# Kernel optimization log

Measured on AMD Instinct MI355X. Metric: run time of the kernel, lower is better.

The kernel has to match this reference:

```python
import jax, jax.numpy as jnp
import numpy as np

BS, QLEN, DIM, H = 2, 2048, 2048, 16
DH = DIM // H


def setup_inputs() -> dict:
    key = jax.random.key(0)
    ks = jax.random.split(key, 10)
    s = 0.02
    return {
        "input": jax.random.normal(ks[0], (BS, QLEN, DIM), jnp.float32),
        "mask": jnp.ones((BS, QLEN), jnp.int32),
        "wq": jax.random.normal(ks[1], (DIM, DIM), jnp.float32) * s,
        "bq": jax.random.normal(ks[2], (DIM,), jnp.float32) * s,
        "wk": jax.random.normal(ks[3], (DIM, DIM), jnp.float32) * s,
        "bk": jax.random.normal(ks[4], (DIM,), jnp.float32) * s,
        "wv": jax.random.normal(ks[5], (DIM, DIM), jnp.float32) * s,
        "bv": jax.random.normal(ks[6], (DIM,), jnp.float32) * s,
        "wo": jax.random.normal(ks[7], (DIM, DIM), jnp.float32) * s,
        "bo": jax.random.normal(ks[8], (DIM,), jnp.float32) * s,
    }


def _shape(x, bs):
    # (bs, len, dim) -> (bs, H, len, DH)
    return x.reshape(bs, -1, H, DH).transpose(0, 2, 1, 3)


def reference(input, mask, wq, bq, wk, bk, wv, bv, wo, bo):
    bs, qlen, dim = input.shape
    # torch Linear: y = x @ W.T + b
    q = _shape(input @ wq.T + bq, bs)  # (bs,H,q,dh)
    k = _shape(input @ wk.T + bk, bs)  # (bs,H,k,dh)
    v = _shape(input @ wv.T + bv, bs)  # (bs,H,k,dh)
    q = q / jnp.sqrt(jnp.asarray(DH, q.dtype))
    scores = jnp.einsum("bhqd,bhkd->bhqk", q, k)
    # mask (bs, klen): positions where mask==0 are masked with -inf
    neg = (mask == 0)[:, None, None, :]  # (bs,1,1,klen)
    scores = jnp.where(neg, -jnp.inf, scores)
    weights = jax.nn.softmax(scores.astype(jnp.float32), axis=-1).astype(scores.dtype)
    # dropout p=0 (eval): identity
    context = jnp.einsum("bhqk,bhkd->bhqd", weights, v)
    context = context.transpose(0, 2, 1, 3).reshape(bs, qlen, dim)
    return context @ wo.T + bo
```

## Files before the change

### kernel.cpp

```cpp
#include <hip/hip_runtime.h>
#include <hip/hip_bf16.h>

#define BS 2
#define QLEN 2048
#define DIM 2048
#define H 16
#define DH 128
#define MTOT (BS*QLEN)

#define BM 256
#define BN 128
#define BK 64
#define NT (DIM/BK)

typedef __hip_bfloat16 bf16;
using f32x4 = __attribute__((ext_vector_type(4))) float;
using s16x8 = __attribute__((ext_vector_type(8))) short;

__device__ inline void gload_lds16(const bf16* g, bf16* l) {
    __builtin_amdgcn_global_load_lds(
        (const __attribute__((address_space(1))) void*)g,
        (__attribute__((address_space(3))) void*)l,
        16, 0, 0);
}

__global__ __launch_bounds__(256) void cast6(
    const float* __restrict__ x,
    const float* __restrict__ w0, const float* __restrict__ w1,
    const float* __restrict__ w2, const float* __restrict__ w3,
    bf16* xo, bf16* o0, bf16* o1, bf16* o2, bf16* o3, int n4)
{
    const float* in; bf16* out;
    switch (blockIdx.y) {
        case 0:  in = w0; out = o0; break;
        case 1:  in = w1; out = o1; break;
        case 2:  in = w2; out = o2; break;
        case 3:  in = w3; out = o3; break;
        case 4:  in = x;        out = xo;        break;
        default: in = x + 4*(size_t)n4; out = xo + 4*(size_t)n4; break;
    }
    int i = blockIdx.x * 256 + threadIdx.x;
    if (i < n4) {
        float4 v = ((const float4*)in)[i];
        __hip_bfloat162 p0 = __float22bfloat162_rn(make_float2(v.x, v.y));
        __hip_bfloat162 p1 = __float22bfloat162_rn(make_float2(v.z, v.w));
        ((__hip_bfloat162*)out)[2*i]   = p0;
        ((__hip_bfloat162*)out)[2*i+1] = p1;
    }
}

__global__ __launch_bounds__(512, 2) void gemm_qk(
    const bf16* __restrict__ A,
    const bf16* __restrict__ Wq, const bf16* __restrict__ Wk,
    const float* __restrict__ bq, const float* __restrict__ bk,
    bf16* __restrict__ Qo, bf16* __restrict__ Ko,
    float qscale)
{
    __shared__ __align__(16) bf16 smem[2*256*64*2];
    bf16* const SA = smem;
    bf16* const SB = smem + 2*256*64;

    const int t = threadIdx.x;
    const int lane = t & 63, w = t >> 6;
    const int row16 = lane & 15, quad = lane >> 4;

    const int sid = (blockIdx.z * 16 + blockIdx.y) * 8 + blockIdx.x;
    const int swz = (sid & 7) * 32 + (sid >> 3);
    const int zz = swz >> 7;
    const int m0 = ((swz >> 3) & 15) * 256;
    const int n0 = (swz & 7) * 256;
    const int mo = (w >> 2) * 128, no = (w & 3) * 64;

    const bf16*  Bw   = (zz == 0) ? Wq : Wk;
    const float* bias = (zz == 0) ? bq : bk;
    const float  scale = (zz == 0) ? qscale : 1.0f;

    auto stageA_part = [&](int kt, int bufi, int h) {
        bf16* dst = SA + bufi * (256*64);
        #pragma unroll
        for (int i = 0; i < 2; i++) {
            int c = i*512 + t;
            int rp = c >> 3, g = c & 7;
            int row = (rp & 63) + ((rp & 64) << 1) + h*64;
            int src = g ^ (row & 7);
            gload_lds16(A + (size_t)(m0 + row) * DIM + kt + src*8, dst + (row*8 + g)*8);
        }
    };
    auto stageB_half = [&](int kt, int bufi, int h) {
        bf16* dst = SB + bufi * (256*64);
        #pragma unroll
        for (int i = 0; i < 2; i++) {
            int c = i*512 + t;
            int rp = c >> 3, g = c & 7;
            int row = rp + h*128;
            int src = g ^ (row & 7);
            gload_lds16(Bw + (size_t)(n0 + row) * DIM + kt + src*8, dst + (row*8 + g)*8);
        }
    };

    f32x4 acc[8][4];
    #pragma unroll
    for (int i = 0; i < 8; i++)
        #pragma unroll
        for (int j = 0; j < 4; j++)
            acc[i][j] = (f32x4){0.f, 0.f, 0.f, 0.f};

    stageB_half(0, 0, 0); stageB_half(0, 0, 1);
    stageA_part(0, 0, 0); stageA_part(0, 0, 1);
    asm volatile("s_waitcnt vmcnt(0)" ::: "memory");
    __builtin_amdgcn_s_barrier();
    asm volatile("" ::: "memory");

    for (int J = 0; J < NT; ++J) {
        const bf16* Asb = SA + (J & 1) * (256*64);
        const bf16* Bsb = SB + (J & 1) * (256*64);
        const int stbuf = (J + 1) & 1;
        const bool st = (J + 1 < NT);
        s16x8 bfr[4][2];

        #pragma unroll
        for (int p = 0; p < 4; ++p) {
            s16x8 af[2][2];
            #pragma unroll
            for (int i = 0; i < 2; i++)
                #pragma unroll
                for (int kk = 0; kk < 2; kk++)
                    af[i][kk] = *(const s16x8*)&Asb[(mo + (2*p+i)*16 + row16)*64 +
                                                    (((kk*4+quad) ^ (row16&7)))*8];
            if (p == 0) {
                #pragma unroll
                for (int nj = 0; nj < 4; nj++)
                    #pragma unroll
                    for (int kk = 0; kk < 2; kk++)
                        bfr[nj][kk] = *(const s16x8*)&Bsb[(no + nj*16 + row16)*64 +
                                                          (((kk*4+quad) ^ (row16&7)))*8];
            }
            if (st) {
                if      (p == 0) stageB_half((J+1)*BK, stbuf, 0);
                else if (p == 1) stageB_half((J+1)*BK, stbuf, 1);
                else if (p == 2) stageA_part((J+1)*BK, stbuf, 0);
                else             stageA_part((J+1)*BK, stbuf, 1);
            }
            if (p == 1) {
                if (J < NT-1) asm volatile("s_waitcnt vmcnt(4)" ::: "memory");
                else          asm volatile("s_waitcnt vmcnt(0)" ::: "memory");
            }
            if (p == 3 && J < NT-1)
                asm volatile("s_waitcnt vmcnt(2)" ::: "memory");

            asm volatile("" ::: "memory");
            __builtin_amdgcn_s_barrier();
            asm volatile("s_waitcnt lgkmcnt(0)" ::: "memory");
            __builtin_amdgcn_sched_barrier(0);
            __builtin_amdgcn_s_setprio(1);
            #pragma unroll
            for (int kk = 0; kk < 2; kk++)
                #pragma unroll
                for (int i = 0; i < 2; i++)
                    #pragma unroll
                    for (int nj = 0; nj < 4; nj++)
                        acc[2*p+i][nj] = __builtin_amdgcn_mfma_f32_16x16x32_bf16(
                            af[i][kk], bfr[nj][kk], acc[2*p+i][nj], 0, 0, 0);
            __builtin_amdgcn_s_setprio(0);
            if (!(p == 3 && J == NT-1)) {
                asm volatile("" ::: "memory");
                __builtin_amdgcn_s_barrier();
                asm volatile("" ::: "memory");
            }
        }
    }

    bf16* out = (zz == 0) ? Qo : Ko;
    #pragma unroll
    for (int mi = 0; mi < 8; mi++)
        #pragma unroll
        for (int nj = 0; nj < 4; nj++) {
            int n = n0 + no + nj*16 + row16;
            float bv_ = bias[n];
            #pragma unroll
            for (int r = 0; r < 4; r++) {
                int m = m0 + mo + mi*16 + quad*4 + r;
                out[(size_t)m * DIM + n] = __float2bfloat16((acc[mi][nj][r] + bv_) * scale);
            }
        }
}

__global__ __launch_bounds__(512, 2) void gemm_v(
    const bf16* __restrict__ A, const bf16* __restrict__ B,
    const float* __restrict__ bias, bf16* __restrict__ Vo)
{
    __shared__ __align__(16) bf16 smem[3*BM*BK + 3*BN*BK];
    bf16* const SA = smem;
    bf16* const SB = smem + 3*BM*BK;

    const int t = threadIdx.x;
    const int lane = t & 63, w = t >> 6;
    const int row16 = lane & 15, quad = lane >> 4;
    const int sid = blockIdx.y * gridDim.x + blockIdx.x;
    const int swz = (sid & 7) * 32 + (sid >> 3);
    const int m0 = (swz >> 4) * BM, n0 = (swz & 15) * BN;
    const int mo = (w >> 1) * 64, no = (w & 1) * 64;

    auto stageA = [&](int kt, int bufi) {
        bf16* dst = SA + bufi * (BM*BK);
        #pragma unroll
        for (int i = 0; i < 4; i++) {
            int idx = i*512 + t;
            int row = idx >> 3, g = idx & 7;
            int src = g ^ (row & 7);
            gload_lds16(A + (size_t)(m0 + row) * DIM + kt + src*8, dst + idx*8);
        }
    };
    auto stageB = [&](int kt, int bufi) {
        bf16* dst = SB + bufi * (BN*BK);
        #pragma unroll
        for (int i = 0; i < 2; i++) {
            int idx = i*512 + t;
            int row = idx >> 3, g = idx & 7;
            int src = g ^ (row & 7);
            gload_lds16(B + (size_t)(n0 + row) * DIM + kt + src*8, dst + idx*8);
        }
    };

    f32x4 acc[4][4];
    for (int i = 0; i < 4; i++)
        for (int j = 0; j < 4; j++)
            acc[i][j] = (f32x4){0.f, 0.f, 0.f, 0.f};

    stageA(0,    0); stageB(0,    0);
    stageA(BK,   1); stageB(BK,   1);
    stageA(2*BK, 2); stageB(2*BK, 2);
    asm volatile("s_waitcnt vmcnt(12)" ::: "memory");
    __builtin_amdgcn_s_barrier();
    asm volatile("" ::: "memory");

    int buf = 0;
    for (int J = 0; J < NT; ++J) {
        const bf16* Asb = SA + buf * (BM*BK);
        const bf16* Bsb = SB + buf * (BN*BK);

        s16x8 af0[4], bf0[4];
        #pragma unroll
        for (int mt = 0; mt < 4; mt++)
            af0[mt] = *(const s16x8*)&Asb[(mo + mt*16 + row16)*BK + ((quad ^ (row16&7)))*8];
        #pragma unroll
        for (int nt = 0; nt < 4; nt++)
            bf0[nt] = *(const s16x8*)&Bsb[(no + nt*16 + row16)*BK + ((quad ^ (row16&7)))*8];
        if (J >= 1 && J + 2 < NT) {
            int sl = (buf == 0) ? 2 : buf - 1;
            stageA((J+2)*BK, sl); stageB((J+2)*BK, sl);
        }
        asm volatile("" ::: "memory");
        __builtin_amdgcn_s_barrier();
        asm volatile("s_waitcnt lgkmcnt(0)" ::: "memory");
        __builtin_amdgcn_sched_barrier(0);
        __builtin_amdgcn_s_setprio(1);
        #pragma unroll
        for (int mt = 0; mt < 4; mt++)
            #pragma unroll
            for (int nt = 0; nt < 4; nt++)
                acc[mt][nt] = __builtin_amdgcn_mfma_f32_16x16x32_bf16(
                    af0[mt], bf0[nt], acc[mt][nt], 0, 0, 0);
        __builtin_amdgcn_s_setprio(0);
        asm volatile("" ::: "memory");
        __builtin_amdgcn_s_barrier();
        asm volatile("" ::: "memory");

        s16x8 af1[4], bf1[4];
        #pragma unroll
        for (int mt = 0; mt < 4; mt++)
            af1[mt] = *(const s16x8*)&Asb[(mo + mt*16 + row16)*BK + (((4+quad) ^ (row16&7)))*8];
        #pragma unroll
        for (int nt = 0; nt < 4; nt++)
            bf1[nt] = *(const s16x8*)&Bsb[(no + nt*16 + row16)*BK + (((4+quad) ^ (row16&7)))*8];
        asm volatile("" ::: "memory");
        __builtin_amdgcn_s_barrier();
        asm volatile("s_waitcnt lgkmcnt(0)" ::: "memory");
        __builtin_amdgcn_sched_barrier(0);
        __builtin_amdgcn_s_setprio(1);
        #pragma unroll
        for (int mt = 0; mt < 4; mt++)
            #pragma unroll
            for (int nt = 0; nt < 4; nt++)
                acc[mt][nt] = __builtin_amdgcn_mfma_f32_16x16x32_bf16(
                    af1[mt], bf1[nt], acc[mt][nt], 0, 0, 0);
        __builtin_amdgcn_s_setprio(0);
        if (J < NT-2)
            asm volatile("s_waitcnt vmcnt(6)" ::: "memory");
        else if (J == NT-2)
            asm volatile("s_waitcnt vmcnt(0)" ::: "memory");
        if (J < NT-1) {
            asm volatile("" ::: "memory");
            __builtin_amdgcn_s_barrier();
            asm volatile("" ::: "memory");
        }
        buf = (buf == 2) ? 0 : buf + 1;
    }

    __syncthreads();
    bf16* Ts = smem;
    for (int mt = 0; mt < 4; mt++)
        for (int nt = 0; nt < 4; nt++) {
            int nn = no + nt*16 + row16;
            float bv_ = bias[n0 + nn];
            for (int r = 0; r < 4; r++) {
                int mm = mo + mt*16 + quad*4 + r;
                Ts[nn*264 + mm] = __float2bfloat16(acc[mt][nt][r] + bv_);
            }
        }
    __syncthreads();
    const int b = m0 >> 11, q0b = m0 & 2047;
    #pragma unroll
    for (int i = 0; i < 8; i++) {
        int chunk = i*512 + t;
        int row = chunk >> 5;
        int c = chunk & 31;
        s16x8 val = *(const s16x8*)&Ts[row*264 + c*8];
        *(s16x8*)(Vo + ((size_t)(b*DIM + n0 + row))*QLEN + q0b + c*8) = val;
    }
}

__global__ __launch_bounds__(512, 2) void gemm_out(
    const bf16* __restrict__ A, const bf16* __restrict__ B,
    const float* __restrict__ bias, float* __restrict__ out)
{
    __shared__ __align__(16) bf16 smem[3*BM*BK + 3*BN*BK];
    bf16* const SA = smem;
    bf16* const SB = smem + 3*BM*BK;

    const int t = threadIdx.x;
    const int lane = t & 63, w = t >> 6;
    const int row16 = lane & 15, quad = lane >> 4;
    const int sid = blockIdx.y * gridDim.x + blockIdx.x;
    const int swz = (sid & 7) * 32 + (sid >> 3);
    const int m0 = (swz >> 4) * BM, n0 = (swz & 15) * BN;
    const int mo = (w >> 1) * 64, no = (w & 1) * 64;

    auto stageA = [&](int kt, int bufi) {
        bf16* dst = SA + bufi * (BM*BK);
        #pragma unroll
        for (int i = 0; i < 4; i++) {
            int idx = i*512 + t;
            int row = idx >> 3, g = idx & 7;
            int src = g ^ (row & 7);
            gload_lds16(A + (size_t)(m0 + row) * DIM + kt + src*8, dst + idx*8);
        }
    };
    auto stageB = [&](int kt, int bufi) {
        bf16* dst = SB + bufi * (BN*BK);
        #pragma unroll
        for (int i = 0; i < 2; i++) {
            int idx = i*512 + t;
            int row = idx >> 3, g = idx & 7;
            int src = g ^ (row & 7);
            gload_lds16(B + (size_t)(n0 + row) * DIM + kt + src*8, dst + idx*8);
        }
    };

    f32x4 acc[4][4];
    for (int i = 0; i < 4; i++)
        for (int j = 0; j < 4; j++)
            acc[i][j] = (f32x4){0.f, 0.f, 0.f, 0.f};

    stageA(0,    0); stageB(0,    0);
    stageA(BK,   1); stageB(BK,   1);
    stageA(2*BK, 2); stageB(2*BK, 2);
    asm volatile("s_waitcnt vmcnt(12)" ::: "memory");
    __builtin_amdgcn_s_barrier();
    asm volatile("" ::: "memory");

    int buf = 0;
    for (int J = 0; J < NT; ++J) {
        const bf16* Asb = SA + buf * (BM*BK);
        const bf16* Bsb = SB + buf * (BN*BK);

        s16x8 af0[4], bf0[4];
        #pragma unroll
        for (int mt = 0; mt < 4; mt++)
            af0[mt] = *(const s16x8*)&Asb[(mo + mt*16 + row16)*BK + ((quad ^ (row16&7)))*8];
        #pragma unroll
        for (int nt = 0; nt < 4; nt++)
            bf0[nt] = *(const s16x8*)&Bsb[(no + nt*16 + row16)*BK + ((quad ^ (row16&7)))*8];
        if (J >= 1 && J + 2 < NT) {
            int sl = (buf == 0) ? 2 : buf - 1;
            stageA((J+2)*BK, sl); stageB((J+2)*BK, sl);
        }
        asm volatile("" ::: "memory");
        __builtin_amdgcn_s_barrier();
        asm volatile("s_waitcnt lgkmcnt(0)" ::: "memory");
        __builtin_amdgcn_sched_barrier(0);
        __builtin_amdgcn_s_setprio(1);
        #pragma unroll
        for (int mt = 0; mt < 4; mt++)
            #pragma unroll
            for (int nt = 0; nt < 4; nt++)
                acc[mt][nt] = __builtin_amdgcn_mfma_f32_16x16x32_bf16(
                    af0[mt], bf0[nt], acc[mt][nt], 0, 0, 0);
        __builtin_amdgcn_s_setprio(0);
        asm volatile("" ::: "memory");
        __builtin_amdgcn_s_barrier();
        asm volatile("" ::: "memory");

        s16x8 af1[4], bf1[4];
        #pragma unroll
        for (int mt = 0; mt < 4; mt++)
            af1[mt] = *(const s16x8*)&Asb[(mo + mt*16 + row16)*BK + (((4+quad) ^ (row16&7)))*8];
        #pragma unroll
        for (int nt = 0; nt < 4; nt++)
            bf1[nt] = *(const s16x8*)&Bsb[(no + nt*16 + row16)*BK + (((4+quad) ^ (row16&7)))*8];
        asm volatile("" ::: "memory");
        __builtin_amdgcn_s_barrier();
        asm volatile("s_waitcnt lgkmcnt(0)" ::: "memory");
        __builtin_amdgcn_sched_barrier(0);
        __builtin_amdgcn_s_setprio(1);
        #pragma unroll
        for (int mt = 0; mt < 4; mt++)
            #pragma unroll
            for (int nt = 0; nt < 4; nt++)
                acc[mt][nt] = __builtin_amdgcn_mfma_f32_16x16x32_bf16(
                    af1[mt], bf1[nt], acc[mt][nt], 0, 0, 0);
        __builtin_amdgcn_s_setprio(0);
        if (J < NT-2)
            asm volatile("s_waitcnt vmcnt(6)" ::: "memory");
        else if (J == NT-2)
            asm volatile("s_waitcnt vmcnt(0)" ::: "memory");
        if (J < NT-1) {
            asm volatile("" ::: "memory");
            __builtin_amdgcn_s_barrier();
            asm volatile("" ::: "memory");
        }
        buf = (buf == 2) ? 0 : buf + 1;
    }

    for (int mt = 0; mt < 4; mt++)
        for (int nt = 0; nt < 4; nt++) {
            int n = n0 + no + nt*16 + row16;
            float bv_ = bias[n];
            for (int r = 0; r < 4; r++) {
                int m = m0 + mo + mt*16 + quad*4 + r;
                out[(size_t)m * DIM + n] = acc[mt][nt][r] + bv_;
            }
        }
}

__global__ __launch_bounds__(256, 2) void attn(
    const bf16* __restrict__ Q, const bf16* __restrict__ Kb,
    const bf16* __restrict__ Vt, const int* __restrict__ mask,
    bf16* __restrict__ Ctx)
{
    __shared__ __align__(16) bf16 Ks[2][64*128];
    __shared__ __align__(16) bf16 Vs[128*64];
    __shared__ __align__(16) bf16 Pl[4][32*64];

    const int t = threadIdx.x, w = t >> 6, lane = t & 63;
    const int row16 = lane & 15, quad = lane >> 4;
    const int sid = blockIdx.y * gridDim.x + blockIdx.x;
    const int swz = (sid & 7) * 64 + (sid >> 3);
    const int bh = swz >> 4, b = bh >> 4, h = bh & 15;
    const int q0 = (swz & 15) * 128 + w * 32;

    s16x8 qf[2][4];
    for (int qs = 0; qs < 2; qs++) {
        const bf16* qp = Q + (size_t)(b*QLEN + q0 + qs*16 + row16) * DIM + h*DH;
        for (int ks = 0; ks < 4; ks++)
            qf[qs][ks] = *(const s16x8*)(qp + ks*32 + quad*8);
    }

    f32x4 o[2][8];
    for (int qs = 0; qs < 2; qs++)
        for (int i = 0; i < 8; i++) o[qs][i] = (f32x4){0.f, 0.f, 0.f, 0.f};
    float lsum[2][4] = {{0.f,0.f,0.f,0.f},{0.f,0.f,0.f,0.f}};
    const int* mrow = mask + b * QLEN;

    const bf16* Kbase = Kb + (size_t)b*QLEN*DIM + h*DH;
    const bf16* Vbase = Vt + ((size_t)b*DIM + h*DH) * QLEN;

    #pragma unroll
    for (int i = 0; i < 4; i++) {
        int idx = i*256 + t;
        int kr = idx >> 4, kc = idx & 15;
        int kg = kc ^ (kr & 15);
        gload_lds16(Kbase + (size_t)kr * DIM + kg*8, &Ks[0][idx*8]);
    }

    for (int it = 0; it < QLEN/64; it++) {
        const int kt = it * 64, buf = it & 1;
        __syncthreads();

        if (it + 1 < QLEN/64) {
            #pragma unroll
            for (int i = 0; i < 4; i++) {
                int idx = i*256 + t;
                int kr = idx >> 4, kc = idx & 15;
                int kg = kc ^ (kr & 15);
                gload_lds16(Kbase + (size_t)(kt + 64 + kr) * DIM + kg*8, &Ks[buf^1][idx*8]);
            }
        }
        #pragma unroll
        for (int i = 0; i < 4; i++) {
            int idx = i*256 + t;
            int vd = idx >> 3, vc = idx & 7;
            int vg = vc ^ (vd & 7);
            gload_lds16(Vbase + (size_t)vd * QLEN + kt + vg*8, &Vs[idx*8]);
        }

        float mval[4];
        #pragma unroll
        for (int nt = 0; nt < 4; nt++)
            mval[nt] = (mrow[kt + nt*16 + row16] != 0) ? -20.0f : -1e30f;

        f32x4 sc[2][4];
        for (int qs = 0; qs < 2; qs++)
            for (int nt = 0; nt < 4; nt++) sc[qs][nt] = (f32x4){0.f, 0.f, 0.f, 0.f};
        #pragma unroll
        for (int ks = 0; ks < 4; ks++) {
            #pragma unroll
            for (int nt = 0; nt < 4; nt++) {
                int rrow = nt*16 + row16;
                int c = (ks*4 + quad) ^ row16;
                s16x8 kf = *(const s16x8*)&Ks[buf][rrow*128 + c*8];
                sc[0][nt] = __builtin_amdgcn_mfma_f32_16x16x32_bf16(qf[0][ks], kf, sc[0][nt], 0, 0, 0);
                sc[1][nt] = __builtin_amdgcn_mfma_f32_16x16x32_bf16(qf[1][ks], kf, sc[1][nt], 0, 0, 0);
            }
        }

        #pragma unroll
        for (int qs = 0; qs < 2; qs++) {
            #pragma unroll
            for (int r = 0; r < 4; r++) {
                int prow = qs*16 + quad*4 + r;
                float ts = 0.f;
                #pragma unroll
                for (int nt = 0; nt < 4; nt++) {
                    float p = exp2f(sc[qs][nt][r] + mval[nt]);
                    ts += p;
                    int chunk = nt*2 + (row16 >> 3);
                    int slot = chunk ^ (prow & 7);
                    Pl[w][prow*64 + slot*8 + (row16 & 7)] = __float2bfloat16(p);
                }
                lsum[qs][r] += ts;
            }
        }

        __syncthreads();

        #pragma unroll
        for (int kc = 0; kc < 2; kc++) {
            int pslot0 = ((kc*4 + quad) ^ (row16 & 7));
            s16x8 pf0 = *(const s16x8*)&Pl[w][(0*16 + row16)*64 + pslot0*8];
            s16x8 pf1 = *(const s16x8*)&Pl[w][(1*16 + row16)*64 + pslot0*8];
            #pragma unroll
            for (int nt = 0; nt < 8; nt++) {
                int d = nt*16 + row16;
                int c = (kc*4 + quad) ^ (d & 7);
                s16x8 vf = *(const s16x8*)&Vs[d*64 + c*8];
                o[0][nt] = __builtin_amdgcn_mfma_f32_16x16x32_bf16(pf0, vf, o[0][nt], 0, 0, 0);
                o[1][nt] = __builtin_amdgcn_mfma_f32_16x16x32_bf16(pf1, vf, o[1][nt], 0, 0, 0);
            }
        }
    }

    for (int qs = 0; qs < 2; qs++) {
        float inv[4];
        for (int r = 0; r < 4; r++) {
            float ts = lsum[qs][r];
            ts += __shfl_xor(ts, 1);
            ts += __shfl_xor(ts, 2);
            ts += __shfl_xor(ts, 4);
            ts += __shfl_xor(ts, 8);
            inv[r] = 1.0f / ts;
        }
        for (int nt = 0; nt < 8; nt++)
            for (int r = 0; r < 4; r++) {
                float v = o[qs][nt][r] * inv[r];
                Ctx[(size_t)(b*QLEN + q0 + qs*16 + quad*4 + r) * DIM + h*DH + nt*16 + row16] =
                    __float2bfloat16(v);
            }
    }
}

extern "C" void kernel_launch(void* const* d_in, const int* in_sizes, int n_in,
                              void* d_out, int out_size, void* d_ws, size_t ws_size,
                              hipStream_t stream) {
    const float* x    = (const float*)d_in[0];
    const int*   mask = (const int*)d_in[1];
    const float* wq   = (const float*)d_in[2];
    const float* bq   = (const float*)d_in[3];
    const float* wk   = (const float*)d_in[4];
    const float* bk   = (const float*)d_in[5];
    const float* wv   = (const float*)d_in[6];
    const float* bv   = (const float*)d_in[7];
    const float* wo   = (const float*)d_in[8];
    const float* bo   = (const float*)d_in[9];

    char* ws = (char*)d_ws;
    const size_t MB = 1024 * 1024;
    bf16* Xb  = (bf16*)(ws);
    bf16* Qb  = (bf16*)(ws + 16*MB);
    bf16* Kb  = (bf16*)(ws + 32*MB);
    bf16* Vtb = (bf16*)(ws + 48*MB);
    bf16* Wqb = (bf16*)(ws + 64*MB);
    bf16* Wkb = (bf16*)(ws + 72*MB);
    bf16* Wvb = (bf16*)(ws + 80*MB);
    bf16* Wob = (bf16*)(ws + 88*MB);
    bf16* Ctx = Xb;

    int n4w = (DIM*DIM) / 4;
    cast6<<<dim3(n4w/256, 6), 256, 0, stream>>>(x, wq, wk, wv, wo,
                                                Xb, Wqb, Wkb, Wvb, Wob, n4w);

    const float qscale = 0.08838834764831845f * 1.4426950408889634f;
    gemm_qk<<<dim3(8, 16, 2), 512, 0, stream>>>(
        Xb, Wqb, Wkb, bq, bk, Qb, Kb, qscale);

    gemm_v<<<dim3(DIM/BN, MTOT/BM), 512, 0, stream>>>(Xb, Wvb, bv, Vtb);

    attn<<<dim3(QLEN/128, BS*H), 256, 0, stream>>>(Qb, Kb, Vtb, mask, Ctx);

    gemm_out<<<dim3(DIM/BN, MTOT/BM), 512, 0, stream>>>(Ctx, Wob, bo, (float*)d_out);
}
```

Baseline: 394.7 us.

## Shrink attention tile to 16 query rows per wave and raise occupancy

Each wave in the attention kernel now handles 16 query rows instead of 32, so each block covers 64 queries and the grid doubles. K staging drops to a single buffer, loaded after the barrier that precedes PV and overlapped with that step, using manual s_waitcnt and barriers. s_setprio is raised around the MFMA sections. The aim is higher occupancy (launch bounds 4) and lower LDS/register use, at the cost of reloading K/V tiles twice as many times per head and less reuse of each loaded tile.

After: 402.8 us. +2.0%, slower.

```diff
diff --git a/kernel.cpp b/kernel.cpp
--- a/kernel.cpp
+++ b/kernel.cpp
@@ -443,59 +443,49 @@
         }
 }
 
-__global__ __launch_bounds__(256, 2) void attn(
+__global__ __launch_bounds__(256, 4) void attn(
     const bf16* __restrict__ Q, const bf16* __restrict__ Kb,
     const bf16* __restrict__ Vt, const int* __restrict__ mask,
     bf16* __restrict__ Ctx)
 {
-    __shared__ __align__(16) bf16 Ks[2][64*128];
+    __shared__ __align__(16) bf16 Ks[64*128];
     __shared__ __align__(16) bf16 Vs[128*64];
-    __shared__ __align__(16) bf16 Pl[4][32*64];
+    __shared__ __align__(16) bf16 Pl[4][16*64];
 
     const int t = threadIdx.x, w = t >> 6, lane = t & 63;
     const int row16 = lane & 15, quad = lane >> 4;
     const int sid = blockIdx.y * gridDim.x + blockIdx.x;
-    const int swz = (sid & 7) * 64 + (sid >> 3);
-    const int bh = swz >> 4, b = bh >> 4, h = bh & 15;
-    const int q0 = (swz & 15) * 128 + w * 32;
-
-    s16x8 qf[2][4];
-    for (int qs = 0; qs < 2; qs++) {
-        const bf16* qp = Q + (size_t)(b*QLEN + q0 + qs*16 + row16) * DIM + h*DH;
+    const int swz = (sid & 7) * 128 + (sid >> 3);
+    const int bh = swz >> 5, b = bh >> 4, h = bh & 15;
+    const int q0 = (swz & 31) * 64 + w * 16;
+
+    s16x8 qf[4];
+    {
+        const bf16* qp = Q + (size_t)(b*QLEN + q0 + row16) * DIM + h*DH;
+        #pragma unroll
         for (int ks = 0; ks < 4; ks++)
-            qf[qs][ks] = *(const s16x8*)(qp + ks*32 + quad*8);
-    }
-
-    f32x4 o[2][8];
-    for (int qs = 0; qs < 2; qs++)
-        for (int i = 0; i < 8; i++) o[qs][i] = (f32x4){0.f, 0.f, 0.f, 0.f};
-    float lsum[2][4] = {{0.f,0.f,0.f,0.f},{0.f,0.f,0.f,0.f}};
+            qf[ks] = *(const s16x8*)(qp + ks*32 + quad*8);
+    }
+
+    f32x4 o[8];
+    #pragma unroll
+    for (int i = 0; i < 8; i++) o[i] = (f32x4){0.f, 0.f, 0.f, 0.f};
+    float lsum[4] = {0.f, 0.f, 0.f, 0.f};
     const int* mrow = mask + b * QLEN;
 
     const bf16* Kbase = Kb + (size_t)b*QLEN*DIM + h*DH;
     const bf16* Vbase = Vt + ((size_t)b*DIM + h*DH) * QLEN;
 
-    #pragma unroll
-    for (int i = 0; i < 4; i++) {
-        int idx = i*256 + t;
-        int kr = idx >> 4, kc = idx & 15;
-        int kg = kc ^ (kr & 15);
-        gload_lds16(Kbase + (size_t)kr * DIM + kg*8, &Ks[0][idx*8]);
-    }
-
-    for (int it = 0; it < QLEN/64; it++) {
-        const int kt = it * 64, buf = it & 1;
-        __syncthreads();
-
-        if (it + 1 < QLEN/64) {
-            #pragma unroll
-            for (int i = 0; i < 4; i++) {
-                int idx = i*256 + t;
-                int kr = idx >> 4, kc = idx & 15;
-                int kg = kc ^ (kr & 15);
-                gload_lds16(Kbase + (size_t)(kt + 64 + kr) * DIM + kg*8, &Ks[buf^1][idx*8]);
-            }
-        }
+    auto stageK = [&](int kt) {
+        #pragma unroll
+        for (int i = 0; i < 4; i++) {
+            int idx = i*256 + t;
+            int kr = idx >> 4, kc = idx & 15;
+            int kg = kc ^ (kr & 15);
+            gload_lds16(Kbase + (size_t)(kt + kr) * DIM + kg*8, &Ks[idx*8]);
+        }
+    };
+    auto stageV = [&](int kt) {
         #pragma unroll
         for (int i = 0; i < 4; i++) {
             int idx = i*256 + t;
@@ -503,80 +493,100 @@
             int vg = vc ^ (vd & 7);
             gload_lds16(Vbase + (size_t)vd * QLEN + kt + vg*8, &Vs[idx*8]);
         }
+    };
+
+    stageK(0);
+
+    for (int it = 0; it < QLEN/64; it++) {
+        const int kt = it * 64;
+
+        asm volatile("" ::: "memory");
+        __builtin_amdgcn_s_barrier();
+        asm volatile("" ::: "memory");
+
+        stageV(kt);
+        asm volatile("s_waitcnt vmcnt(4)" ::: "memory");
+        __builtin_amdgcn_s_barrier();
+        asm volatile("" ::: "memory");
 
         float mval[4];
         #pragma unroll
         for (int nt = 0; nt < 4; nt++)
             mval[nt] = (mrow[kt + nt*16 + row16] != 0) ? -20.0f : -1e30f;
 
-        f32x4 sc[2][4];
-        for (int qs = 0; qs < 2; qs++)
-            for (int nt = 0; nt < 4; nt++) sc[qs][nt] = (f32x4){0.f, 0.f, 0.f, 0.f};
+        f32x4 sc[4];
+        #pragma unroll
+        for (int nt = 0; nt < 4; nt++) sc[nt] = (f32x4){0.f, 0.f, 0.f, 0.f};
+        __builtin_amdgcn_s_setprio(1);
         #pragma unroll
         for (int ks = 0; ks < 4; ks++) {
             #pragma unroll
             for (int nt = 0; nt < 4; nt++) {
                 int rrow = nt*16 + row16;
                 int c = (ks*4 + quad) ^ row16;
-                s16x8 kf = *(const s16x8*)&Ks[buf][rrow*128 + c*8];
-                sc[0][nt] = __builtin_amdgcn_mfma_f32_16x16x32_bf16(qf[0][ks], kf, sc[0][nt], 0, 0, 0);
-                sc[1][nt] = __builtin_amdgcn_mfma_f32_16x16x32_bf16(qf[1][ks], kf, sc[1][nt], 0, 0, 0);
-            }
-        }
-
-        #pragma unroll
-        for (int qs = 0; qs < 2; qs++) {
-            #pragma unroll
-            for (int r = 0; r < 4; r++) {
-                int prow = qs*16 + quad*4 + r;
-                float ts = 0.f;
-                #pragma unroll
-                for (int nt = 0; nt < 4; nt++) {
-                    float p = exp2f(sc[qs][nt][r] + mval[nt]);
-                    ts += p;
-                    int chunk = nt*2 + (row16 >> 3);
-                    int slot = chunk ^ (prow & 7);
-                    Pl[w][prow*64 + slot*8 + (row16 & 7)] = __float2bfloat16(p);
-                }
-                lsum[qs][r] += ts;
-            }
-        }
-
-        __syncthreads();
-
+                s16x8 kf = *(const s16x8*)&Ks[rrow*128 + c*8];
+                sc[nt] = __builtin_amdgcn_mfma_f32_16x16x32_bf16(qf[ks], kf, sc[nt], 0, 0, 0);
+            }
+        }
+        __builtin_amdgcn_s_setprio(0);
+
+        #pragma unroll
+        for (int r = 0; r < 4; r++) {
+            int prow = quad*4 + r;
+            float ts = 0.f;
+            #pragma unroll
+            for (int nt = 0; nt < 4; nt++) {
+                float p = exp2f(sc[nt][r] + mval[nt]);
+                ts += p;
+                int chunk = nt*2 + (row16 >> 3);
+                int slot = chunk ^ (prow & 7);
+                Pl[w][prow*64 + slot*8 + (row16 & 7)] = __float2bfloat16(p);
+            }
+            lsum[r] += ts;
+        }
+
+        asm volatile("s_waitcnt lgkmcnt(0)" ::: "memory");
+        asm volatile("s_waitcnt vmcnt(0)" ::: "memory");
+        __builtin_amdgcn_s_barrier();
+        asm volatile("" ::: "memory");
+
+        if (it + 1 < QLEN/64)
+            stageK(kt + 64);
+
+        __builtin_amdgcn_s_setprio(1);
         #pragma unroll
         for (int kc = 0; kc < 2; kc++) {
             int pslot0 = ((kc*4 + quad) ^ (row16 & 7));
-            s16x8 pf0 = *(const s16x8*)&Pl[w][(0*16 + row16)*64 + pslot0*8];
-            s16x8 pf1 = *(const s16x8*)&Pl[w][(1*16 + row16)*64 + pslot0*8];
+            s16x8 pf = *(const s16x8*)&Pl[w][row16*64 + pslot0*8];
             #pragma unroll
             for (int nt = 0; nt < 8; nt++) {
                 int d = nt*16 + row16;
                 int c = (kc*4 + quad) ^ (d & 7);
                 s16x8 vf = *(const s16x8*)&Vs[d*64 + c*8];
-                o[0][nt] = __builtin_amdgcn_mfma_f32_16x16x32_bf16(pf0, vf, o[0][nt], 0, 0, 0);
-                o[1][nt] = __builtin_amdgcn_mfma_f32_16x16x32_bf16(pf1, vf, o[1][nt], 0, 0, 0);
-            }
-        }
-    }
-
-    for (int qs = 0; qs < 2; qs++) {
-        float inv[4];
+                o[nt] = __builtin_amdgcn_mfma_f32_16x16x32_bf16(pf, vf, o[nt], 0, 0, 0);
+            }
+        }
+        __builtin_amdgcn_s_setprio(0);
+    }
+
+    float inv[4];
+    #pragma unroll
+    for (int r = 0; r < 4; r++) {
+        float ts = lsum[r];
+        ts += __shfl_xor(ts, 1);
+        ts += __shfl_xor(ts, 2);
+        ts += __shfl_xor(ts, 4);
+        ts += __shfl_xor(ts, 8);
+        inv[r] = 1.0f / ts;
+    }
+    #pragma unroll
+    for (int nt = 0; nt < 8; nt++)
+        #pragma unroll
         for (int r = 0; r < 4; r++) {
-            float ts = lsum[qs][r];
-            ts += __shfl_xor(ts, 1);
-            ts += __shfl_xor(ts, 2);
-            ts += __shfl_xor(ts, 4);
-            ts += __shfl_xor(ts, 8);
-            inv[r] = 1.0f / ts;
-        }
-        for (int nt = 0; nt < 8; nt++)
-            for (int r = 0; r < 4; r++) {
-                float v = o[qs][nt][r] * inv[r];
-                Ctx[(size_t)(b*QLEN + q0 + qs*16 + quad*4 + r) * DIM + h*DH + nt*16 + row16] =
-                    __float2bfloat16(v);
-            }
-    }
+            float v = o[nt][r] * inv[r];
+            Ctx[(size_t)(b*QLEN + q0 + quad*4 + r) * DIM + h*DH + nt*16 + row16] =
+                __float2bfloat16(v);
+        }
 }
 
 extern "C" void kernel_launch(void* const* d_in, const int* in_sizes, int n_in,
@@ -615,7 +625,7 @@
 
     gemm_v<<<dim3(DIM/BN, MTOT/BM), 512, 0, stream>>>(Xb, Wvb, bv, Vtb);
 
-    attn<<<dim3(QLEN/128, BS*H), 256, 0, stream>>>(Qb, Kb, Vtb, mask, Ctx);
+    attn<<<dim3(QLEN/64, BS*H), 256, 0, stream>>>(Qb, Kb, Vtb, mask, Ctx);
 
     gemm_out<<<dim3(DIM/BN, MTOT/BM), 512, 0, stream>>>(Ctx, Wob, bo, (float*)d_out);
 }
```

## Double-buffer V tile and prefetch K/V one iteration ahead in attention

Applied to the files above, without the earlier changes.

The attention kernel now double-buffers the V tile alongside K, so both next tiles are issued before computing the current one. Explicit vmcnt waits let the current tile's loads complete while the next tile's loads stay in flight. The mid-iteration block barrier becomes a per-wave lgkmcnt wait plus a sched barrier, since P is private per wave. s_setprio raises priority around the MFMA sections. LDS use grows by 16KB per block, which may lower occupancy below the two-blocks-per-CU launch bound.

After: 391.7 us. About the same (-0.8%).

```diff
diff --git a/kernel.cpp b/kernel.cpp
--- a/kernel.cpp
+++ b/kernel.cpp
@@ -449,7 +449,7 @@
     bf16* __restrict__ Ctx)
 {
     __shared__ __align__(16) bf16 Ks[2][64*128];
-    __shared__ __align__(16) bf16 Vs[128*64];
+    __shared__ __align__(16) bf16 Vs[2][128*64];
     __shared__ __align__(16) bf16 Pl[4][32*64];
 
     const int t = threadIdx.x, w = t >> 6, lane = t & 63;
@@ -475,34 +475,45 @@
     const bf16* Kbase = Kb + (size_t)b*QLEN*DIM + h*DH;
     const bf16* Vbase = Vt + ((size_t)b*DIM + h*DH) * QLEN;
 
-    #pragma unroll
-    for (int i = 0; i < 4; i++) {
-        int idx = i*256 + t;
-        int kr = idx >> 4, kc = idx & 15;
-        int kg = kc ^ (kr & 15);
-        gload_lds16(Kbase + (size_t)kr * DIM + kg*8, &Ks[0][idx*8]);
-    }
-
-    for (int it = 0; it < QLEN/64; it++) {
-        const int kt = it * 64, buf = it & 1;
-        __syncthreads();
-
-        if (it + 1 < QLEN/64) {
-            #pragma unroll
-            for (int i = 0; i < 4; i++) {
-                int idx = i*256 + t;
-                int kr = idx >> 4, kc = idx & 15;
-                int kg = kc ^ (kr & 15);
-                gload_lds16(Kbase + (size_t)(kt + 64 + kr) * DIM + kg*8, &Ks[buf^1][idx*8]);
-            }
-        }
+    auto stageK = [&](int kt, int bi) {
+        #pragma unroll
+        for (int i = 0; i < 4; i++) {
+            int idx = i*256 + t;
+            int kr = idx >> 4, kc = idx & 15;
+            int kg = kc ^ (kr & 15);
+            gload_lds16(Kbase + (size_t)(kt + kr) * DIM + kg*8, &Ks[bi][idx*8]);
+        }
+    };
+    auto stageV = [&](int kt, int bi) {
         #pragma unroll
         for (int i = 0; i < 4; i++) {
             int idx = i*256 + t;
             int vd = idx >> 3, vc = idx & 7;
             int vg = vc ^ (vd & 7);
-            gload_lds16(Vbase + (size_t)vd * QLEN + kt + vg*8, &Vs[idx*8]);
-        }
+            gload_lds16(Vbase + (size_t)vd * QLEN + kt + vg*8, &Vs[bi][idx*8]);
+        }
+    };
+
+    stageK(0, 0);
+    stageV(0, 0);
+
+    for (int it = 0; it < QLEN/64; it++) {
+        const int kt = it * 64, buf = it & 1;
+
+        asm volatile("" ::: "memory");
+        __builtin_amdgcn_s_barrier();
+        asm volatile("" ::: "memory");
+
+        if (it + 1 < QLEN/64) {
+            stageK(kt + 64, buf ^ 1);
+            stageV(kt + 64, buf ^ 1);
+            asm volatile("s_waitcnt vmcnt(8)" ::: "memory");
+        } else {
+            asm volatile("s_waitcnt vmcnt(0)" ::: "memory");
+        }
+        asm volatile("" ::: "memory");
+        __builtin_amdgcn_s_barrier();
+        asm volatile("" ::: "memory");
 
         float mval[4];
         #pragma unroll
@@ -512,6 +523,7 @@
         f32x4 sc[2][4];
         for (int qs = 0; qs < 2; qs++)
             for (int nt = 0; nt < 4; nt++) sc[qs][nt] = (f32x4){0.f, 0.f, 0.f, 0.f};
+        __builtin_amdgcn_s_setprio(1);
         #pragma unroll
         for (int ks = 0; ks < 4; ks++) {
             #pragma unroll
@@ -523,6 +535,7 @@
                 sc[1][nt] = __builtin_amdgcn_mfma_f32_16x16x32_bf16(qf[1][ks], kf, sc[1][nt], 0, 0, 0);
             }
         }
+        __builtin_amdgcn_s_setprio(0);
 
         #pragma unroll
         for (int qs = 0; qs < 2; qs++) {
@@ -542,8 +555,10 @@
             }
         }
 
-        __syncthreads();
-
+        asm volatile("s_waitcnt lgkmcnt(0)" ::: "memory");
+        __builtin_amdgcn_sched_barrier(0);
+
+        __builtin_amdgcn_s_setprio(1);
         #pragma unroll
         for (int kc = 0; kc < 2; kc++) {
             int pslot0 = ((kc*4 + quad) ^ (row16 & 7));
@@ -553,11 +568,12 @@
             for (int nt = 0; nt < 8; nt++) {
                 int d = nt*16 + row16;
                 int c = (kc*4 + quad) ^ (d & 7);
-                s16x8 vf = *(const s16x8*)&Vs[d*64 + c*8];
+                s16x8 vf = *(const s16x8*)&Vs[buf][d*64 + c*8];
                 o[0][nt] = __builtin_amdgcn_mfma_f32_16x16x32_bf16(pf0, vf, o[0][nt], 0, 0, 0);
                 o[1][nt] = __builtin_amdgcn_mfma_f32_16x16x32_bf16(pf1, vf, o[1][nt], 0, 0, 0);
             }
         }
+        __builtin_amdgcn_s_setprio(0);
     }
 
     for (int qs = 0; qs < 2; qs++) {
```
